# Kernel tuning notes

Hardware: AMD Instinct MI355X
Metric: run time of the kernel (lower is better)

The kernel has to match this reference:

```python
import jax, jax.numpy as jnp
import numpy as np

NUM_USERS = 100000
NUM_ITEMS = 50000
EMBED = 64
S_NNZ = NUM_USERS * 32   # avg social degree 32
R_NNZ = NUM_USERS * 50   # avg 50 rated items per user
BATCH = 8192


def setup_inputs() -> dict:
    key = jax.random.key(0)
    ks = jax.random.split(key, 12)
    d = EMBED
    # Embedding tables (xavier-uniform style scale)
    U = jax.random.uniform(ks[0], (NUM_USERS, d), jnp.float32, -1.0, 1.0) * np.sqrt(6.0 / (NUM_USERS + d))
    V = jax.random.uniform(ks[1], (NUM_ITEMS, d), jnp.float32, -1.0, 1.0) * np.sqrt(6.0 / (NUM_ITEMS + d))
    # Diffusion layer weights: Linear(2d -> d). Stored as [2d, d] (x @ W + b).
    lim = np.sqrt(6.0 / (3 * d))
    W0 = jax.random.uniform(ks[2], (2 * d, d), jnp.float32, -lim, lim)
    b0 = jnp.zeros((d,), jnp.float32)
    W1 = jax.random.uniform(ks[3], (2 * d, d), jnp.float32, -lim, lim)
    b1 = jnp.zeros((d,), jnp.float32)
    # Sparse social matrix S [NUM_USERS, NUM_USERS], COO edge lists, row-normalized values.
    S_row = jax.random.randint(ks[4], (S_NNZ,), 0, NUM_USERS, jnp.int32)
    S_col = jax.random.randint(ks[5], (S_NNZ,), 0, NUM_USERS, jnp.int32)
    S_val = jnp.full((S_NNZ,), 1.0 / 32.0, jnp.float32)
    # Sparse rating matrix R [NUM_USERS, NUM_ITEMS]
    R_row = jax.random.randint(ks[6], (R_NNZ,), 0, NUM_USERS, jnp.int32)
    R_col = jax.random.randint(ks[7], (R_NNZ,), 0, NUM_ITEMS, jnp.int32)
    R_val = jnp.full((R_NNZ,), 1.0 / 50.0, jnp.float32)
    batch_user = jax.random.randint(ks[8], (BATCH,), 0, NUM_USERS, jnp.int64 if jax.config.jax_enable_x64 else jnp.int32)
    batch_pos_item = jax.random.randint(ks[9], (BATCH,), 0, NUM_ITEMS, jnp.int32)
    batch_neg_item = jax.random.randint(ks[10], (BATCH,), 0, NUM_ITEMS, jnp.int32)
    return dict(batch_user=batch_user, batch_pos_item=batch_pos_item, batch_neg_item=batch_neg_item,
                U=U, V=V, W0=W0, b0=b0, W1=W1, b1=b1,
                S_row=S_row, S_col=S_col, S_val=S_val,
                R_row=R_row, R_col=R_col, R_val=R_val)


def _spmm(row, col, val, X, n_rows):
    # (sparse [n_rows, n] COO) @ X : gather + scale + segment-sum
    return jax.ops.segment_sum(val[:, None] * X[col], row, num_segments=n_rows)


def reference(batch_user, batch_pos_item, batch_neg_item, U, V, W0, b0, W1, b1,
              S_row, S_col, S_val, R_row, R_col, R_val):
    # Diffusion layers: U <- relu(concat([S @ U, U]) @ W + b)
    for W, b in ((W0, b0), (W1, b1)):
        agg = _spmm(S_row, S_col, S_val, U, NUM_USERS)          # [num_users, d]
        U = jax.nn.relu(jnp.concatenate([agg, U], axis=1) @ W + b)
    user_g = U + _spmm(R_row, R_col, R_val, V, NUM_USERS)        # [num_users, d]
    bu = user_g[batch_user]          # [B, d]
    bp = V[batch_pos_item]           # [B, d]
    bn = V[batch_neg_item]           # [B, d]
    return (bu, bp, bn)
```

## Files before the change

### kernel.cpp

```cpp
#include <hip/hip_runtime.h>
#include <hip/hip_bf16.h>

#define NUM_USERS 100000
#define NUM_ITEMS 50000
#define EMBED     64
#define S_NNZ     (NUM_USERS * 32)
#define R_NNZ     (NUM_USERS * 50)
#define BATCH     8192

#define NB    256
#define NCH   256
#define CHUNK (S_NNZ / NCH)
#define BROWS 391

#define SEGCAP 160


__global__ __launch_bounds__(256) void k_p1hist(const int* __restrict__ rows, int* __restrict__ cnt_t,
                                                int* __restrict__ head, unsigned* __restrict__ bitmap,
                                                int* __restrict__ cntR) {
    __shared__ int h[NB];
    int t = threadIdx.x, b = blockIdx.x;
    int gid = b * 256 + t;
    for (int i = gid; i < NUM_USERS; i += NB * 256) head[i] = -1;
    for (int i = gid; i < (NUM_USERS + 31) / 32; i += NB * 256) bitmap[i] = 0;
    for (int i = gid; i < BATCH; i += NB * 256) cntR[i] = 0;
    h[t] = 0;
    __syncthreads();
    int base = b * CHUNK;
    for (int i = t; i < CHUNK; i += 256) atomicAdd(&h[rows[base + i] / BROWS], 1);
    __syncthreads();
    cnt_t[t * NCH + b] = h[t];
}

__global__ __launch_bounds__(1024) void k_scan1(const int* __restrict__ cnt, int* __restrict__ excl,
                                                int* __restrict__ bsums, int n) {
    __shared__ int buf[1024];
    int t = threadIdx.x;
    int i = blockIdx.x * 1024 + t;
    int x = (i < n) ? cnt[i] : 0;
    buf[t] = x;
    __syncthreads();
    for (int off = 1; off < 1024; off <<= 1) {
        int y = (t >= off) ? buf[t - off] : 0;
        __syncthreads();
        buf[t] += y;
        __syncthreads();
    }
    if (i < n) excl[i] = buf[t] - x;
    if (t == 1023) bsums[blockIdx.x] = buf[1023];
}

__global__ __launch_bounds__(1024) void k_scan2(int* __restrict__ bsums, int nb, int* __restrict__ total_slot) {
    __shared__ int buf[1024];
    int t = threadIdx.x;
    int x = (t < nb) ? bsums[t] : 0;
    buf[t] = x;
    __syncthreads();
    for (int off = 1; off < 1024; off <<= 1) {
        int y = (t >= off) ? buf[t - off] : 0;
        __syncthreads();
        buf[t] += y;
        __syncthreads();
    }
    if (t < nb) bsums[t] = buf[t] - x;
    if (t == 1023) total_slot[0] = buf[1023];
}

__global__ void k_scan3b(int* __restrict__ a, const int* __restrict__ bsums, int n) {
    int i = blockIdx.x * blockDim.x + threadIdx.x;
    if (i < n) a[i] += bsums[i >> 10];
}

__global__ __launch_bounds__(256) void k_p1scatter(const int* __restrict__ rows, const int* __restrict__ cols,
                                                   const float* __restrict__ vals, const int* __restrict__ cnt_t,
                                                   int2* __restrict__ tmpE) {
    __shared__ int cur[NB];
    int t = threadIdx.x, b = blockIdx.x;
    cur[t] = cnt_t[t * NCH + b];
    __syncthreads();
    int base = b * CHUNK;
    for (int i = t; i < CHUNK; i += 256) {
        int e  = base + i;
        int r  = rows[e];
        int bk = r / BROWS;
        int pos = atomicAdd(&cur[bk], 1);
        tmpE[pos] = make_int2(((r - bk * BROWS) << 17) | cols[e], __float_as_int(vals[e]));
    }
}

__global__ __launch_bounds__(512) void k_p2(const int2* __restrict__ tmpE, const int* __restrict__ cnt_t,
                                            int* __restrict__ rowptr, int2* __restrict__ colval) {
    __shared__ int h[512];
    __shared__ int s[512];
    __shared__ int cur[512];
    int t = threadIdx.x, k = blockIdx.x;
    int beg = cnt_t[k * NCH];
    int end = (k < NB - 1) ? cnt_t[(k + 1) * NCH] : S_NNZ;
    h[t] = 0;
    __syncthreads();
    for (int j = beg + t; j < end; j += 512) atomicAdd(&h[((unsigned)tmpE[j].x) >> 17], 1);
    __syncthreads();
    s[t] = h[t];
    __syncthreads();
    for (int off = 1; off < 512; off <<= 1) {
        int y = (t >= off) ? s[t - off] : 0;
        __syncthreads();
        s[t] += y;
        __syncthreads();
    }
    int excl = s[t] - h[t];
    int gr   = k * BROWS + t;
    if (t <= BROWS && gr <= NUM_USERS) rowptr[gr] = beg + excl;
    cur[t] = beg + excl;
    __syncthreads();
    for (int j = beg + t; j < end; j += 512) {
        int2 e  = tmpE[j];
        int pos = atomicAdd(&cur[((unsigned)e.x) >> 17], 1);
        colval[pos] = make_int2(e.x & 0x1FFFF, e.y);
    }
}

__global__ void k_cvt(const float* __restrict__ src, __hip_bfloat16* __restrict__ dst, int n) {
    int i = blockIdx.x * blockDim.x + threadIdx.x;
    if (i < n) dst[i] = __float2bfloat16(src[i]);
}

__global__ __launch_bounds__(256) void k_spmm16(const int* __restrict__ rowptr,
                                                const int2* __restrict__ colval,
                                                const __hip_bfloat16* __restrict__ X,
                                                float* __restrict__ Y, int n_rows) {
    int w    = blockIdx.x * (blockDim.x >> 6) + (threadIdx.x >> 6);
    int lane = threadIdx.x & 63;
    if (w >= n_rows) return;
    int beg = rowptr[w], end = rowptr[w + 1];
    float acc = 0.0f;
    int j    = beg;
    int jend = beg + ((end - beg) & ~7);
    for (; j < jend; j += 8) {
        int2 cv[8];
#pragma unroll
        for (int u = 0; u < 8; ++u) cv[u] = colval[j + u];
        float x[8];
#pragma unroll
        for (int u = 0; u < 8; ++u) x[u] = __bfloat162float(X[(size_t)cv[u].x * EMBED + lane]);
#pragma unroll
        for (int u = 0; u < 8; ++u) acc = fmaf(__int_as_float(cv[u].y), x[u], acc);
    }
    for (; j < end; ++j)
        acc = fmaf(__int_as_float(colval[j].y), __bfloat162float(X[(size_t)colval[j].x * EMBED + lane]), acc);
    Y[(size_t)w * EMBED + lane] = acc;
}

__global__ __launch_bounds__(256) void k_spmm_batch16(const int* __restrict__ rowptr,
                                                      const int2* __restrict__ colval,
                                                      const __hip_bfloat16* __restrict__ X,
                                                      const int* __restrict__ bu,
                                                      float* __restrict__ Agg2, int n) {
    int w    = blockIdx.x * (blockDim.x >> 6) + (threadIdx.x >> 6);
    int lane = threadIdx.x & 63;
    if (w >= n) return;
    int r   = bu[w];
    int beg = rowptr[r], end = rowptr[r + 1];
    float acc = 0.0f;
    int j    = beg;
    int jend = beg + ((end - beg) & ~7);
    for (; j < jend; j += 8) {
        int2 cv[8];
#pragma unroll
        for (int u = 0; u < 8; ++u) cv[u] = colval[j + u];
        float x[8];
#pragma unroll
        for (int u = 0; u < 8; ++u) x[u] = __bfloat162float(X[(size_t)cv[u].x * EMBED + lane]);
#pragma unroll
        for (int u = 0; u < 8; ++u) acc = fmaf(__int_as_float(cv[u].y), x[u], acc);
    }
    for (; j < end; ++j)
        acc = fmaf(__int_as_float(colval[j].y), __bfloat162float(X[(size_t)colval[j].x * EMBED + lane]), acc);
    Agg2[(size_t)w * EMBED + lane] = acc;
}


__global__ __launch_bounds__(256) void k_layer(const float* __restrict__ Agg,
                                               const float* __restrict__ Uin,
                                               float* __restrict__ Uout,
                                               __hip_bfloat16* __restrict__ Uout16,
                                               const float* __restrict__ W,
                                               const float* __restrict__ b) {
    __shared__ __align__(16) float Wt[64 * 128];
    int t = threadIdx.x;
    for (int i = t; i < 128 * 64; i += 256) {
        int k = i >> 6, c = i & 63;
        Wt[c * 128 + ((((k >> 2) ^ (c & 7)) << 2) | (k & 3))] = W[i];
    }
    int rl = __builtin_amdgcn_readfirstlane(t >> 6);
    int c  = t & 63;
    int rbase = blockIdx.x * 16 + rl * 4;
    __syncthreads();
    const float4* Wt4 = (const float4*)Wt;
    int  csw   = c & 7;
    int  cbase = c * 32;
    const float4* a0 = (const float4*)(Agg + (size_t)(rbase + 0) * EMBED);
    const float4* a1 = (const float4*)(Agg + (size_t)(rbase + 1) * EMBED);
    const float4* a2 = (const float4*)(Agg + (size_t)(rbase + 2) * EMBED);
    const float4* a3 = (const float4*)(Agg + (size_t)(rbase + 3) * EMBED);
    const float4* u0 = (const float4*)(Uin + (size_t)(rbase + 0) * EMBED);
    const float4* u1 = (const float4*)(Uin + (size_t)(rbase + 1) * EMBED);
    const float4* u2 = (const float4*)(Uin + (size_t)(rbase + 2) * EMBED);
    const float4* u3 = (const float4*)(Uin + (size_t)(rbase + 3) * EMBED);
    float bias = b[c];
    float acc0 = bias, acc1 = bias, acc2 = bias, acc3 = bias;
#pragma unroll 4
    for (int k4 = 0; k4 < 16; ++k4) {
        float4 w4 = Wt4[cbase + (k4 ^ csw)];
        float4 x0 = a0[k4], x1 = a1[k4], x2 = a2[k4], x3 = a3[k4];
        acc0 = fmaf(x0.x, w4.x, acc0); acc0 = fmaf(x0.y, w4.y, acc0); acc0 = fmaf(x0.z, w4.z, acc0); acc0 = fmaf(x0.w, w4.w, acc0);
        acc1 = fmaf(x1.x, w4.x, acc1); acc1 = fmaf(x1.y, w4.y, acc1); acc1 = fmaf(x1.z, w4.z, acc1); acc1 = fmaf(x1.w, w4.w, acc1);
        acc2 = fmaf(x2.x, w4.x, acc2); acc2 = fmaf(x2.y, w4.y, acc2); acc2 = fmaf(x2.z, w4.z, acc2); acc2 = fmaf(x2.w, w4.w, acc2);
        acc3 = fmaf(x3.x, w4.x, acc3); acc3 = fmaf(x3.y, w4.y, acc3); acc3 = fmaf(x3.z, w4.z, acc3); acc3 = fmaf(x3.w, w4.w, acc3);
    }
#pragma unroll 4
    for (int k4 = 16; k4 < 32; ++k4) {
        float4 w4 = Wt4[cbase + (k4 ^ csw)];
        float4 x0 = u0[k4 - 16], x1 = u1[k4 - 16], x2 = u2[k4 - 16], x3 = u3[k4 - 16];
        acc0 = fmaf(x0.x, w4.x, acc0); acc0 = fmaf(x0.y, w4.y, acc0); acc0 = fmaf(x0.z, w4.z, acc0); acc0 = fmaf(x0.w, w4.w, acc0);
        acc1 = fmaf(x1.x, w4.x, acc1); acc1 = fmaf(x1.y, w4.y, acc1); acc1 = fmaf(x1.z, w4.z, acc1); acc1 = fmaf(x1.w, w4.w, acc1);
        acc2 = fmaf(x2.x, w4.x, acc2); acc2 = fmaf(x2.y, w4.y, acc2); acc2 = fmaf(x2.z, w4.z, acc2); acc2 = fmaf(x2.w, w4.w, acc2);
        acc3 = fmaf(x3.x, w4.x, acc3); acc3 = fmaf(x3.y, w4.y, acc3); acc3 = fmaf(x3.z, w4.z, acc3); acc3 = fmaf(x3.w, w4.w, acc3);
    }
    float v0 = fmaxf(acc0, 0.0f), v1 = fmaxf(acc1, 0.0f), v2 = fmaxf(acc2, 0.0f), v3 = fmaxf(acc3, 0.0f);
    Uout[(size_t)(rbase + 0) * EMBED + c] = v0;
    Uout[(size_t)(rbase + 1) * EMBED + c] = v1;
    Uout[(size_t)(rbase + 2) * EMBED + c] = v2;
    Uout[(size_t)(rbase + 3) * EMBED + c] = v3;
    Uout16[(size_t)(rbase + 0) * EMBED + c] = __float2bfloat16(v0);
    Uout16[(size_t)(rbase + 1) * EMBED + c] = __float2bfloat16(v1);
    Uout16[(size_t)(rbase + 2) * EMBED + c] = __float2bfloat16(v2);
    Uout16[(size_t)(rbase + 3) * EMBED + c] = __float2bfloat16(v3);
}

__global__ __launch_bounds__(256) void k_layer_batch(const float* __restrict__ Agg2,
                                                     const float* __restrict__ Uin,
                                                     const int* __restrict__ bu,
                                                     float* __restrict__ out0,
                                                     const float* __restrict__ W,
                                                     const float* __restrict__ b,
                                                     const float* __restrict__ V,
                                                     const int* __restrict__ bp,
                                                     const int* __restrict__ bn) {
    __shared__ __align__(16) float Wt[64 * 128];
    int t = threadIdx.x;
    for (int i = t; i < 128 * 64; i += 256) {
        int k = i >> 6, c = i & 63;
        Wt[c * 128 + ((((k >> 2) ^ (c & 7)) << 2) | (k & 3))] = W[i];
    }
    int rl = __builtin_amdgcn_readfirstlane(t >> 6);
    int c  = t & 63;
    int sbase = blockIdx.x * 16 + rl * 4;
    int r0 = bu[sbase + 0], r1 = bu[sbase + 1], r2 = bu[sbase + 2], r3 = bu[sbase + 3];
    __syncthreads();
    const float4* Wt4 = (const float4*)Wt;
    int  csw   = c & 7;
    int  cbase = c * 32;
    const float4* a0 = (const float4*)(Agg2 + (size_t)(sbase + 0) * EMBED);
    const float4* a1 = (const float4*)(Agg2 + (size_t)(sbase + 1) * EMBED);
    const float4* a2 = (const float4*)(Agg2 + (size_t)(sbase + 2) * EMBED);
    const float4* a3 = (const float4*)(Agg2 + (size_t)(sbase + 3) * EMBED);
    const float4* u0 = (const float4*)(Uin + (size_t)r0 * EMBED);
    const float4* u1 = (const float4*)(Uin + (size_t)r1 * EMBED);
    const float4* u2 = (const float4*)(Uin + (size_t)r2 * EMBED);
    const float4* u3 = (const float4*)(Uin + (size_t)r3 * EMBED);
    float bias = b[c];
    float acc0 = bias, acc1 = bias, acc2 = bias, acc3 = bias;
#pragma unroll 4
    for (int k4 = 0; k4 < 16; ++k4) {
        float4 w4 = Wt4[cbase + (k4 ^ csw)];
        float4 x0 = a0[k4], x1 = a1[k4], x2 = a2[k4], x3 = a3[k4];
        acc0 = fmaf(x0.x, w4.x, acc0); acc0 = fmaf(x0.y, w4.y, acc0); acc0 = fmaf(x0.z, w4.z, acc0); acc0 = fmaf(x0.w, w4.w, acc0);
        acc1 = fmaf(x1.x, w4.x, acc1); acc1 = fmaf(x1.y, w4.y, acc1); acc1 = fmaf(x1.z, w4.z, acc1); acc1 = fmaf(x1.w, w4.w, acc1);
        acc2 = fmaf(x2.x, w4.x, acc2); acc2 = fmaf(x2.y, w4.y, acc2); acc2 = fmaf(x2.z, w4.z, acc2); acc2 = fmaf(x2.w, w4.w, acc2);
        acc3 = fmaf(x3.x, w4.x, acc3); acc3 = fmaf(x3.y, w4.y, acc3); acc3 = fmaf(x3.z, w4.z, acc3); acc3 = fmaf(x3.w, w4.w, acc3);
    }
#pragma unroll 4
    for (int k4 = 16; k4 < 32; ++k4) {
        float4 w4 = Wt4[cbase + (k4 ^ csw)];
        float4 x0 = u0[k4 - 16], x1 = u1[k4 - 16], x2 = u2[k4 - 16], x3 = u3[k4 - 16];
        acc0 = fmaf(x0.x, w4.x, acc0); acc0 = fmaf(x0.y, w4.y, acc0); acc0 = fmaf(x0.z, w4.z, acc0); acc0 = fmaf(x0.w, w4.w, acc0);
        acc1 = fmaf(x1.x, w4.x, acc1); acc1 = fmaf(x1.y, w4.y, acc1); acc1 = fmaf(x1.z, w4.z, acc1); acc1 = fmaf(x1.w, w4.w, acc1);
        acc2 = fmaf(x2.x, w4.x, acc2); acc2 = fmaf(x2.y, w4.y, acc2); acc2 = fmaf(x2.z, w4.z, acc2); acc2 = fmaf(x2.w, w4.w, acc2);
        acc3 = fmaf(x3.x, w4.x, acc3); acc3 = fmaf(x3.y, w4.y, acc3); acc3 = fmaf(x3.z, w4.z, acc3); acc3 = fmaf(x3.w, w4.w, acc3);
    }
    out0[(size_t)(sbase + 0) * EMBED + c] = fmaxf(acc0, 0.0f);
    out0[(size_t)(sbase + 1) * EMBED + c] = fmaxf(acc1, 0.0f);
    out0[(size_t)(sbase + 2) * EMBED + c] = fmaxf(acc2, 0.0f);
    out0[(size_t)(sbase + 3) * EMBED + c] = fmaxf(acc3, 0.0f);
#pragma unroll
    for (int q = 0; q < 4; ++q) {
        int s = sbase + q;
        out0[(size_t)(BATCH + s) * EMBED + c]     = V[(size_t)bp[s] * EMBED + c];
        out0[(size_t)(2 * BATCH + s) * EMBED + c] = V[(size_t)bn[s] * EMBED + c];
    }
}


__global__ void k_chain(const int* __restrict__ bu, int* __restrict__ head,
                        int* __restrict__ nxt, unsigned* __restrict__ bitmap, int n) {
    int i = blockIdx.x * blockDim.x + threadIdx.x;
    if (i < n) {
        int u = bu[i];
        nxt[i] = atomicExch(&head[u], i);
        atomicOr(&bitmap[u >> 5], 1u << (u & 31));
    }
}

__global__ __launch_bounds__(256) void k_rseg(const int* __restrict__ rows,
                                              const int* __restrict__ cols,
                                              const float* __restrict__ vals,
                                              const unsigned* __restrict__ bitmap,
                                              const int* __restrict__ head,
                                              int* __restrict__ cntR,
                                              int2* __restrict__ seg, int nnz,
                                              const float* __restrict__ V,
                                              __hip_bfloat16* __restrict__ V16) {
    int e = blockIdx.x * blockDim.x + threadIdx.x;
    if (e < NUM_ITEMS * EMBED) V16[e] = __float2bfloat16(V[e]);
    if (e >= nnz) return;
    int r = rows[e];
    if (!((bitmap[(unsigned)r >> 5] >> (r & 31)) & 1u)) return;
    int s   = head[r];
    int pos = atomicAdd(&cntR[s], 1);
    if (pos < SEGCAP) seg[s * SEGCAP + pos] = make_int2(cols[e], __float_as_int(vals[e]));
}

__global__ __launch_bounds__(256) void k_rspmm(const int* __restrict__ cntR,
                                               const int2* __restrict__ seg,
                                               const __hip_bfloat16* __restrict__ V16,
                                               const int* __restrict__ bu,
                                               const int* __restrict__ head,
                                               const int* __restrict__ nxt,
                                               float* __restrict__ out0) {
    int s    = blockIdx.x * (blockDim.x >> 6) + (threadIdx.x >> 6);
    int lane = threadIdx.x & 63;
    if (s >= BATCH) return;
    if (head[bu[s]] != s) return;
    int n = cntR[s];
    if (n > SEGCAP) n = SEGCAP;
    const int2* cv2 = seg + (size_t)s * SEGCAP;
    float acc = 0.0f;
    int j    = 0;
    int jend = n & ~7;
    for (; j < jend; j += 8) {
        int2 cv[8];
#pragma unroll
        for (int u = 0; u < 8; ++u) cv[u] = cv2[j + u];
        float x[8];
#pragma unroll
        for (int u = 0; u < 8; ++u) x[u] = __bfloat162float(V16[(size_t)cv[u].x * EMBED + lane]);
#pragma unroll
        for (int u = 0; u < 8; ++u) acc = fmaf(__int_as_float(cv[u].y), x[u], acc);
    }
    for (; j < n; ++j)
        acc = fmaf(__int_as_float(cv2[j].y), __bfloat162float(V16[(size_t)cv2[j].x * EMBED + lane]), acc);
    int slot = s;
    while (slot >= 0) {
        out0[(size_t)slot * EMBED + lane] += acc;
        slot = nxt[slot];
    }
}


extern "C" void kernel_launch(void* const* d_in, const int* in_sizes, int n_in,
                              void* d_out, int out_size, void* d_ws, size_t ws_size,
                              hipStream_t stream) {
    const int*   batch_user = (const int*)d_in[0];
    const int*   batch_pos  = (const int*)d_in[1];
    const int*   batch_neg  = (const int*)d_in[2];
    const float* U     = (const float*)d_in[3];
    const float* V     = (const float*)d_in[4];
    const float* W0    = (const float*)d_in[5];
    const float* b0    = (const float*)d_in[6];
    const float* W1    = (const float*)d_in[7];
    const float* b1    = (const float*)d_in[8];
    const int*   S_row = (const int*)d_in[9];
    const int*   S_col = (const int*)d_in[10];
    const float* S_val = (const float*)d_in[11];
    const int*   R_row = (const int*)d_in[12];
    const int*   R_col = (const int*)d_in[13];
    const float* R_val = (const float*)d_in[14];
    float* out = (float*)d_out;

    const size_t tabElems = (size_t)NUM_USERS * EMBED;

    char* wsb = (char*)d_ws;
    size_t o = 0;
    float* A       = (float*)(wsb + o); o += tabElems * 4;
    float* B       = (float*)(wsb + o); o += tabElems * 4;
    float* Agg2    = (float*)(wsb + o); o += (size_t)BATCH * EMBED * 4;
    int*   rowptrS = (int*)(wsb + o);   o += (NUM_USERS + 1) * 4;
    int*   cnt_t   = (int*)(wsb + o);   o += (size_t)NB * NCH * 4;
    int*   bsums   = (int*)(wsb + o);   o += 1024 * 4;
    int*   head    = (int*)(wsb + o);   o += NUM_USERS * 4;
    int*   nxt     = (int*)(wsb + o);   o += BATCH * 4;
    int*   cntR    = (int*)(wsb + o);   o += BATCH * 4;
    unsigned* bitmap = (unsigned*)(wsb + o); o += ((NUM_USERS + 31) / 32) * 4;
    o = (o + 7) & ~(size_t)7;
    int2*  colvalS = (int2*)(wsb + o);  o += (size_t)S_NNZ * 8;
    __hip_bfloat16* X16 = (__hip_bfloat16*)(wsb + o); o += tabElems * 2;

    int2* tmpE = (int2*)A;
    int2* seg  = (int2*)B;

    const int spmm_blocks  = (NUM_USERS * 64 + 255) / 256;
    const int layer_blocks = (NUM_USERS + 15) / 16;

    k_p1hist<<<NCH, 256, 0, stream>>>(S_row, cnt_t, head, bitmap, cntR);
    k_scan1<<<(NB * NCH) / 1024, 1024, 0, stream>>>(cnt_t, cnt_t, bsums, NB * NCH);
    k_scan2<<<1, 1024, 0, stream>>>(bsums, (NB * NCH) / 1024, &bsums[512]);
    k_scan3b<<<(NB * NCH) / 256, 256, 0, stream>>>(cnt_t, bsums, NB * NCH);
    k_p1scatter<<<NCH, 256, 0, stream>>>(S_row, S_col, S_val, cnt_t, tmpE);
    k_p2<<<NB, 512, 0, stream>>>(tmpE, cnt_t, rowptrS, colvalS);

    k_cvt<<<(int)((tabElems + 255) / 256), 256, 0, stream>>>(U, X16, (int)tabElems);
    k_spmm16<<<spmm_blocks, 256, 0, stream>>>(rowptrS, colvalS, X16, B, NUM_USERS);
    k_layer<<<layer_blocks, 256, 0, stream>>>(B, U, A, X16, W0, b0);

    k_chain<<<(BATCH + 255) / 256, 256, 0, stream>>>(batch_user, head, nxt, bitmap, BATCH);

    k_spmm_batch16<<<(BATCH * 64 + 255) / 256, 256, 0, stream>>>(rowptrS, colvalS, X16, batch_user, Agg2, BATCH);
    k_layer_batch<<<(BATCH + 15) / 16, 256, 0, stream>>>(Agg2, A, batch_user, out, W1, b1,
                                                         V, batch_pos, batch_neg);

    k_rseg<<<(R_NNZ + 255) / 256, 256, 0, stream>>>(R_row, R_col, R_val, bitmap, head, cntR, seg, R_NNZ,
                                                    V, X16);
    k_rspmm<<<(BATCH * 64 + 255) / 256, 256, 0, stream>>>(cntR, seg, X16, batch_user, head, nxt, out);
}
```

Baseline: 511.6 us.

## Fuse SpMM with dense layer and fold small kernels into preprocessing

Merges the social SpMM and the Linear+ReLU layer into one kernel, for both the full-table layer and the batch-only second layer. Each wave computes the aggregated row, stages it with the input row in LDS, and multiplies by the LDS-resident weight matrix. This removes the fp32 Agg round trip through global memory and several launches. The batch chain-building work is folded into k_scan1 and the fp32-to-bf16 conversion of U into k_p1scatter. The cost is more LDS per block, lower occupancy with 512-thread blocks, and per-row serialization of the gather and the matmul within a wave.

```diff
diff --git a/kernel.cpp b/kernel.cpp
--- a/kernel.cpp
+++ b/kernel.cpp
@@ -34,10 +34,17 @@
 }
 
 __global__ __launch_bounds__(1024) void k_scan1(const int* __restrict__ cnt, int* __restrict__ excl,
-                                                int* __restrict__ bsums, int n) {
-    __shared__ int buf[1024];
+                                                int* __restrict__ bsums, int n,
+                                                const int* __restrict__ bu, int* __restrict__ head,
+                                                int* __restrict__ nxt, unsigned* __restrict__ bitmap) {
     int t = threadIdx.x;
     int i = blockIdx.x * 1024 + t;
+    if (i < BATCH) {
+        int u = bu[i];
+        nxt[i] = atomicExch(&head[u], i);
+        atomicOr(&bitmap[u >> 5], 1u << (u & 31));
+    }
+    __shared__ int buf[1024];
     int x = (i < n) ? cnt[i] : 0;
     buf[t] = x;
     __syncthreads();
@@ -74,7 +81,8 @@
 
 __global__ __launch_bounds__(256) void k_p1scatter(const int* __restrict__ rows, const int* __restrict__ cols,
                                                    const float* __restrict__ vals, const int* __restrict__ cnt_t,
-                                                   int2* __restrict__ tmpE) {
+                                                   int2* __restrict__ tmpE,
+                                                   const float* __restrict__ U, __hip_bfloat16* __restrict__ U16) {
     __shared__ int cur[NB];
     int t = threadIdx.x, b = blockIdx.x;
     cur[t] = cnt_t[t * NCH + b];
@@ -87,6 +95,8 @@
         int pos = atomicAdd(&cur[bk], 1);
         tmpE[pos] = make_int2(((r - bk * BROWS) << 17) | cols[e], __float_as_int(vals[e]));
     }
+    const int total = NUM_USERS * EMBED;
+    for (int i = b * 256 + t; i < total; i += NB * 256) U16[i] = __float2bfloat16(U[i]);
 }
 
 __global__ __launch_bounds__(512) void k_p2(const int2* __restrict__ tmpE, const int* __restrict__ cnt_t,
@@ -121,197 +131,129 @@
     }
 }
 
-__global__ void k_cvt(const float* __restrict__ src, __hip_bfloat16* __restrict__ dst, int n) {
-    int i = blockIdx.x * blockDim.x + threadIdx.x;
-    if (i < n) dst[i] = __float2bfloat16(src[i]);
-}
-
-__global__ __launch_bounds__(256) void k_spmm16(const int* __restrict__ rowptr,
-                                                const int2* __restrict__ colval,
-                                                const __hip_bfloat16* __restrict__ X,
-                                                float* __restrict__ Y, int n_rows) {
-    int w    = blockIdx.x * (blockDim.x >> 6) + (threadIdx.x >> 6);
-    int lane = threadIdx.x & 63;
-    if (w >= n_rows) return;
-    int beg = rowptr[w], end = rowptr[w + 1];
-    float acc = 0.0f;
-    int j    = beg;
-    int jend = beg + ((end - beg) & ~7);
-    for (; j < jend; j += 8) {
-        int2 cv[8];
-#pragma unroll
-        for (int u = 0; u < 8; ++u) cv[u] = colval[j + u];
-        float x[8];
-#pragma unroll
-        for (int u = 0; u < 8; ++u) x[u] = __bfloat162float(X[(size_t)cv[u].x * EMBED + lane]);
-#pragma unroll
-        for (int u = 0; u < 8; ++u) acc = fmaf(__int_as_float(cv[u].y), x[u], acc);
-    }
-    for (; j < end; ++j)
-        acc = fmaf(__int_as_float(colval[j].y), __bfloat162float(X[(size_t)colval[j].x * EMBED + lane]), acc);
-    Y[(size_t)w * EMBED + lane] = acc;
-}
-
-__global__ __launch_bounds__(256) void k_spmm_batch16(const int* __restrict__ rowptr,
-                                                      const int2* __restrict__ colval,
-                                                      const __hip_bfloat16* __restrict__ X,
-                                                      const int* __restrict__ bu,
-                                                      float* __restrict__ Agg2, int n) {
-    int w    = blockIdx.x * (blockDim.x >> 6) + (threadIdx.x >> 6);
-    int lane = threadIdx.x & 63;
-    if (w >= n) return;
-    int r   = bu[w];
-    int beg = rowptr[r], end = rowptr[r + 1];
-    float acc = 0.0f;
-    int j    = beg;
-    int jend = beg + ((end - beg) & ~7);
-    for (; j < jend; j += 8) {
-        int2 cv[8];
-#pragma unroll
-        for (int u = 0; u < 8; ++u) cv[u] = colval[j + u];
-        float x[8];
-#pragma unroll
-        for (int u = 0; u < 8; ++u) x[u] = __bfloat162float(X[(size_t)cv[u].x * EMBED + lane]);
-#pragma unroll
-        for (int u = 0; u < 8; ++u) acc = fmaf(__int_as_float(cv[u].y), x[u], acc);
-    }
-    for (; j < end; ++j)
-        acc = fmaf(__int_as_float(colval[j].y), __bfloat162float(X[(size_t)colval[j].x * EMBED + lane]), acc);
-    Agg2[(size_t)w * EMBED + lane] = acc;
-}
-
-
-__global__ __launch_bounds__(256) void k_layer(const float* __restrict__ Agg,
-                                               const float* __restrict__ Uin,
-                                               float* __restrict__ Uout,
-                                               __hip_bfloat16* __restrict__ Uout16,
-                                               const float* __restrict__ W,
-                                               const float* __restrict__ b) {
-    __shared__ __align__(16) float Wt[64 * 128];
+
+__global__ __launch_bounds__(512) void k_spmm_layer(const int* __restrict__ rowptr,
+                                                    const int2* __restrict__ colval,
+                                                    const __hip_bfloat16* __restrict__ X,
+                                                    const float* __restrict__ Uin,
+                                                    float* __restrict__ Uout,
+                                                    __hip_bfloat16* __restrict__ Uout16,
+                                                    const float* __restrict__ W,
+                                                    const float* __restrict__ b) {
+    __shared__ __align__(16) float Wl[128 * 64];
+    __shared__ __align__(16) float xs[8][128];
     int t = threadIdx.x;
-    for (int i = t; i < 128 * 64; i += 256) {
+    for (int i = t; i < 128 * 64; i += 512) {
         int k = i >> 6, c = i & 63;
-        Wt[c * 128 + ((((k >> 2) ^ (c & 7)) << 2) | (k & 3))] = W[i];
-    }
-    int rl = __builtin_amdgcn_readfirstlane(t >> 6);
-    int c  = t & 63;
-    int rbase = blockIdx.x * 16 + rl * 4;
-    __syncthreads();
-    const float4* Wt4 = (const float4*)Wt;
-    int  csw   = c & 7;
-    int  cbase = c * 32;
-    const float4* a0 = (const float4*)(Agg + (size_t)(rbase + 0) * EMBED);
-    const float4* a1 = (const float4*)(Agg + (size_t)(rbase + 1) * EMBED);
-    const float4* a2 = (const float4*)(Agg + (size_t)(rbase + 2) * EMBED);
-    const float4* a3 = (const float4*)(Agg + (size_t)(rbase + 3) * EMBED);
-    const float4* u0 = (const float4*)(Uin + (size_t)(rbase + 0) * EMBED);
-    const float4* u1 = (const float4*)(Uin + (size_t)(rbase + 1) * EMBED);
-    const float4* u2 = (const float4*)(Uin + (size_t)(rbase + 2) * EMBED);
-    const float4* u3 = (const float4*)(Uin + (size_t)(rbase + 3) * EMBED);
-    float bias = b[c];
-    float acc0 = bias, acc1 = bias, acc2 = bias, acc3 = bias;
-#pragma unroll 4
-    for (int k4 = 0; k4 < 16; ++k4) {
-        float4 w4 = Wt4[cbase + (k4 ^ csw)];
-        float4 x0 = a0[k4], x1 = a1[k4], x2 = a2[k4], x3 = a3[k4];
-        acc0 = fmaf(x0.x, w4.x, acc0); acc0 = fmaf(x0.y, w4.y, acc0); acc0 = fmaf(x0.z, w4.z, acc0); acc0 = fmaf(x0.w, w4.w, acc0);
-        acc1 = fmaf(x1.x, w4.x, acc1); acc1 = fmaf(x1.y, w4.y, acc1); acc1 = fmaf(x1.z, w4.z, acc1); acc1 = fmaf(x1.w, w4.w, acc1);
-        acc2 = fmaf(x2.x, w4.x, acc2); acc2 = fmaf(x2.y, w4.y, acc2); acc2 = fmaf(x2.z, w4.z, acc2); acc2 = fmaf(x2.w, w4.w, acc2);
-        acc3 = fmaf(x3.x, w4.x, acc3); acc3 = fmaf(x3.y, w4.y, acc3); acc3 = fmaf(x3.z, w4.z, acc3); acc3 = fmaf(x3.w, w4.w, acc3);
-    }
-#pragma unroll 4
-    for (int k4 = 16; k4 < 32; ++k4) {
-        float4 w4 = Wt4[cbase + (k4 ^ csw)];
-        float4 x0 = u0[k4 - 16], x1 = u1[k4 - 16], x2 = u2[k4 - 16], x3 = u3[k4 - 16];
-        acc0 = fmaf(x0.x, w4.x, acc0); acc0 = fmaf(x0.y, w4.y, acc0); acc0 = fmaf(x0.z, w4.z, acc0); acc0 = fmaf(x0.w, w4.w, acc0);
-        acc1 = fmaf(x1.x, w4.x, acc1); acc1 = fmaf(x1.y, w4.y, acc1); acc1 = fmaf(x1.z, w4.z, acc1); acc1 = fmaf(x1.w, w4.w, acc1);
-        acc2 = fmaf(x2.x, w4.x, acc2); acc2 = fmaf(x2.y, w4.y, acc2); acc2 = fmaf(x2.z, w4.z, acc2); acc2 = fmaf(x2.w, w4.w, acc2);
-        acc3 = fmaf(x3.x, w4.x, acc3); acc3 = fmaf(x3.y, w4.y, acc3); acc3 = fmaf(x3.z, w4.z, acc3); acc3 = fmaf(x3.w, w4.w, acc3);
-    }
-    float v0 = fmaxf(acc0, 0.0f), v1 = fmaxf(acc1, 0.0f), v2 = fmaxf(acc2, 0.0f), v3 = fmaxf(acc3, 0.0f);
-    Uout[(size_t)(rbase + 0) * EMBED + c] = v0;
-    Uout[(size_t)(rbase + 1) * EMBED + c] = v1;
-    Uout[(size_t)(rbase + 2) * EMBED + c] = v2;
-    Uout[(size_t)(rbase + 3) * EMBED + c] = v3;
-    Uout16[(size_t)(rbase + 0) * EMBED + c] = __float2bfloat16(v0);
-    Uout16[(size_t)(rbase + 1) * EMBED + c] = __float2bfloat16(v1);
-    Uout16[(size_t)(rbase + 2) * EMBED + c] = __float2bfloat16(v2);
-    Uout16[(size_t)(rbase + 3) * EMBED + c] = __float2bfloat16(v3);
-}
-
-__global__ __launch_bounds__(256) void k_layer_batch(const float* __restrict__ Agg2,
-                                                     const float* __restrict__ Uin,
-                                                     const int* __restrict__ bu,
-                                                     float* __restrict__ out0,
-                                                     const float* __restrict__ W,
-                                                     const float* __restrict__ b,
-                                                     const float* __restrict__ V,
-                                                     const int* __restrict__ bp,
-                                                     const int* __restrict__ bn) {
-    __shared__ __align__(16) float Wt[64 * 128];
+        Wl[c * 128 + ((((k >> 2) ^ (c & 7)) << 2) | (k & 3))] = W[i];
+    }
+    __syncthreads();
+    int wv   = t >> 6;
+    int lane = t & 63;
+    int csw  = lane & 7;
+    int cbase = lane * 32;
+    const float4* Wt4 = (const float4*)Wl;
+    float bias = b[lane];
+    int rbase = blockIdx.x * 32 + wv * 4;
+#pragma unroll
+    for (int q = 0; q < 4; ++q) {
+        int row = rbase + q;
+        int beg = rowptr[row], end = rowptr[row + 1];
+        float acc = 0.0f;
+        int j    = beg;
+        int jend = beg + ((end - beg) & ~7);
+        for (; j < jend; j += 8) {
+            int2 cv[8];
+#pragma unroll
+            for (int u = 0; u < 8; ++u) cv[u] = colval[j + u];
+            float x[8];
+#pragma unroll
+            for (int u = 0; u < 8; ++u) x[u] = __bfloat162float(X[(size_t)cv[u].x * EMBED + lane]);
+#pragma unroll
+            for (int u = 0; u < 8; ++u) acc = fmaf(__int_as_float(cv[u].y), x[u], acc);
+        }
+        for (; j < end; ++j)
+            acc = fmaf(__int_as_float(colval[j].y), __bfloat162float(X[(size_t)colval[j].x * EMBED + lane]), acc);
+        xs[wv][lane]      = acc;
+        xs[wv][64 + lane] = Uin[(size_t)row * EMBED + lane];
+        const float4* xv = (const float4*)xs[wv];
+        float accL = bias;
+#pragma unroll 8
+        for (int k4 = 0; k4 < 32; ++k4) {
+            float4 w4 = Wt4[cbase + (k4 ^ csw)];
+            float4 x4 = xv[k4];
+            accL = fmaf(x4.x, w4.x, accL); accL = fmaf(x4.y, w4.y, accL);
+            accL = fmaf(x4.z, w4.z, accL); accL = fmaf(x4.w, w4.w, accL);
+        }
+        float v = fmaxf(accL, 0.0f);
+        Uout[(size_t)row * EMBED + lane]   = v;
+        Uout16[(size_t)row * EMBED + lane] = __float2bfloat16(v);
+    }
+}
+
+__global__ __launch_bounds__(512) void k_spmm_layer_batch(const int* __restrict__ rowptr,
+                                                          const int2* __restrict__ colval,
+                                                          const __hip_bfloat16* __restrict__ X,
+                                                          const float* __restrict__ Uin,
+                                                          const int* __restrict__ bu,
+                                                          float* __restrict__ out0,
+                                                          const float* __restrict__ W,
+                                                          const float* __restrict__ b,
+                                                          const float* __restrict__ V,
+                                                          const int* __restrict__ bp,
+                                                          const int* __restrict__ bn) {
+    __shared__ __align__(16) float Wl[128 * 64];
+    __shared__ __align__(16) float xs[8][128];
     int t = threadIdx.x;
-    for (int i = t; i < 128 * 64; i += 256) {
+    for (int i = t; i < 128 * 64; i += 512) {
         int k = i >> 6, c = i & 63;
-        Wt[c * 128 + ((((k >> 2) ^ (c & 7)) << 2) | (k & 3))] = W[i];
-    }
-    int rl = __builtin_amdgcn_readfirstlane(t >> 6);
-    int c  = t & 63;
-    int sbase = blockIdx.x * 16 + rl * 4;
-    int r0 = bu[sbase + 0], r1 = bu[sbase + 1], r2 = bu[sbase + 2], r3 = bu[sbase + 3];
-    __syncthreads();
-    const float4* Wt4 = (const float4*)Wt;
-    int  csw   = c & 7;
-    int  cbase = c * 32;
-    const float4* a0 = (const float4*)(Agg2 + (size_t)(sbase + 0) * EMBED);
-    const float4* a1 = (const float4*)(Agg2 + (size_t)(sbase + 1) * EMBED);
-    const float4* a2 = (const float4*)(Agg2 + (size_t)(sbase + 2) * EMBED);
-    const float4* a3 = (const float4*)(Agg2 + (size_t)(sbase + 3) * EMBED);
-    const float4* u0 = (const float4*)(Uin + (size_t)r0 * EMBED);
-    const float4* u1 = (const float4*)(Uin + (size_t)r1 * EMBED);
-    const float4* u2 = (const float4*)(Uin + (size_t)r2 * EMBED);
-    const float4* u3 = (const float4*)(Uin + (size_t)r3 * EMBED);
-    float bias = b[c];
-    float acc0 = bias, acc1 = bias, acc2 = bias, acc3 = bias;
-#pragma unroll 4
-    for (int k4 = 0; k4 < 16; ++k4) {
-        float4 w4 = Wt4[cbase + (k4 ^ csw)];
-        float4 x0 = a0[k4], x1 = a1[k4], x2 = a2[k4], x3 = a3[k4];
-        acc0 = fmaf(x0.x, w4.x, acc0); acc0 = fmaf(x0.y, w4.y, acc0); acc0 = fmaf(x0.z, w4.z, acc0); acc0 = fmaf(x0.w, w4.w, acc0);
-        acc1 = fmaf(x1.x, w4.x, acc1); acc1 = fmaf(x1.y, w4.y, acc1); acc1 = fmaf(x1.z, w4.z, acc1); acc1 = fmaf(x1.w, w4.w, acc1);
-        acc2 = fmaf(x2.x, w4.x, acc2); acc2 = fmaf(x2.y, w4.y, acc2); acc2 = fmaf(x2.z, w4.z, acc2); acc2 = fmaf(x2.w, w4.w, acc2);
-        acc3 = fmaf(x3.x, w4.x, acc3); acc3 = fmaf(x3.y, w4.y, acc3); acc3 = fmaf(x3.z, w4.z, acc3); acc3 = fmaf(x3.w, w4.w, acc3);
-    }
-#pragma unroll 4
-    for (int k4 = 16; k4 < 32; ++k4) {
-        float4 w4 = Wt4[cbase + (k4 ^ csw)];
-        float4 x0 = u0[k4 - 16], x1 = u1[k4 - 16], x2 = u2[k4 - 16], x3 = u3[k4 - 16];
-        acc0 = fmaf(x0.x, w4.x, acc0); acc0 = fmaf(x0.y, w4.y, acc0); acc0 = fmaf(x0.z, w4.z, acc0); acc0 = fmaf(x0.w, w4.w, acc0);
-        acc1 = fmaf(x1.x, w4.x, acc1); acc1 = fmaf(x1.y, w4.y, acc1); acc1 = fmaf(x1.z, w4.z, acc1); acc1 = fmaf(x1.w, w4.w, acc1);
-        acc2 = fmaf(x2.x, w4.x, acc2); acc2 = fmaf(x2.y, w4.y, acc2); acc2 = fmaf(x2.z, w4.z, acc2); acc2 = fmaf(x2.w, w4.w, acc2);
-        acc3 = fmaf(x3.x, w4.x, acc3); acc3 = fmaf(x3.y, w4.y, acc3); acc3 = fmaf(x3.z, w4.z, acc3); acc3 = fmaf(x3.w, w4.w, acc3);
-    }
-    out0[(size_t)(sbase + 0) * EMBED + c] = fmaxf(acc0, 0.0f);
-    out0[(size_t)(sbase + 1) * EMBED + c] = fmaxf(acc1, 0.0f);
-    out0[(size_t)(sbase + 2) * EMBED + c] = fmaxf(acc2, 0.0f);
-    out0[(size_t)(sbase + 3) * EMBED + c] = fmaxf(acc3, 0.0f);
+        Wl[c * 128 + ((((k >> 2) ^ (c & 7)) << 2) | (k & 3))] = W[i];
+    }
+    __syncthreads();
+    int wv   = t >> 6;
+    int lane = t & 63;
+    int csw  = lane & 7;
+    int cbase = lane * 32;
+    const float4* Wt4 = (const float4*)Wl;
+    float bias = b[lane];
+    int sbase = blockIdx.x * 32 + wv * 4;
 #pragma unroll
     for (int q = 0; q < 4; ++q) {
         int s = sbase + q;
-        out0[(size_t)(BATCH + s) * EMBED + c]     = V[(size_t)bp[s] * EMBED + c];
-        out0[(size_t)(2 * BATCH + s) * EMBED + c] = V[(size_t)bn[s] * EMBED + c];
-    }
-}
-
-
-__global__ void k_chain(const int* __restrict__ bu, int* __restrict__ head,
-                        int* __restrict__ nxt, unsigned* __restrict__ bitmap, int n) {
-    int i = blockIdx.x * blockDim.x + threadIdx.x;
-    if (i < n) {
-        int u = bu[i];
-        nxt[i] = atomicExch(&head[u], i);
-        atomicOr(&bitmap[u >> 5], 1u << (u & 31));
-    }
-}
+        int r = bu[s];
+        int beg = rowptr[r], end = rowptr[r + 1];
+        float acc = 0.0f;
+        int j    = beg;
+        int jend = beg + ((end - beg) & ~7);
+        for (; j < jend; j += 8) {
+            int2 cv[8];
+#pragma unroll
+            for (int u = 0; u < 8; ++u) cv[u] = colval[j + u];
+            float x[8];
+#pragma unroll
+            for (int u = 0; u < 8; ++u) x[u] = __bfloat162float(X[(size_t)cv[u].x * EMBED + lane]);
+#pragma unroll
+            for (int u = 0; u < 8; ++u) acc = fmaf(__int_as_float(cv[u].y), x[u], acc);
+        }
+        for (; j < end; ++j)
+            acc = fmaf(__int_as_float(colval[j].y), __bfloat162float(X[(size_t)colval[j].x * EMBED + lane]), acc);
+        xs[wv][lane]      = acc;
+        xs[wv][64 + lane] = Uin[(size_t)r * EMBED + lane];
+        const float4* xv = (const float4*)xs[wv];
+        float accL = bias;
+#pragma unroll 8
+        for (int k4 = 0; k4 < 32; ++k4) {
+            float4 w4 = Wt4[cbase + (k4 ^ csw)];
+            float4 x4 = xv[k4];
+            accL = fmaf(x4.x, w4.x, accL); accL = fmaf(x4.y, w4.y, accL);
+            accL = fmaf(x4.z, w4.z, accL); accL = fmaf(x4.w, w4.w, accL);
+        }
+        out0[(size_t)s * EMBED + lane] = fmaxf(accL, 0.0f);
+        out0[(size_t)(BATCH + s) * EMBED + lane]     = V[(size_t)bp[s] * EMBED + lane];
+        out0[(size_t)(2 * BATCH + s) * EMBED + lane] = V[(size_t)bn[s] * EMBED + lane];
+    }
+}
+
 
 __global__ __launch_bounds__(256) void k_rseg(const int* __restrict__ rows,
                                               const int* __restrict__ cols,
@@ -395,7 +337,6 @@
     size_t o = 0;
     float* A       = (float*)(wsb + o); o += tabElems * 4;
     float* B       = (float*)(wsb + o); o += tabElems * 4;
-    float* Agg2    = (float*)(wsb + o); o += (size_t)BATCH * EMBED * 4;
     int*   rowptrS = (int*)(wsb + o);   o += (NUM_USERS + 1) * 4;
     int*   cnt_t   = (int*)(wsb + o);   o += (size_t)NB * NCH * 4;
     int*   bsums   = (int*)(wsb + o);   o += 1024 * 4;
@@ -409,26 +350,20 @@
 
     int2* tmpE = (int2*)A;
     int2* seg  = (int2*)B;
-
-    const int spmm_blocks  = (NUM_USERS * 64 + 255) / 256;
-    const int layer_blocks = (NUM_USERS + 15) / 16;
+    __hip_bfloat16* A16 = (__hip_bfloat16*)((char*)B + tabElems * 2);
 
     k_p1hist<<<NCH, 256, 0, stream>>>(S_row, cnt_t, head, bitmap, cntR);
-    k_scan1<<<(NB * NCH) / 1024, 1024, 0, stream>>>(cnt_t, cnt_t, bsums, NB * NCH);
+    k_scan1<<<(NB * NCH) / 1024, 1024, 0, stream>>>(cnt_t, cnt_t, bsums, NB * NCH,
+                                                    batch_user, head, nxt, bitmap);
     k_scan2<<<1, 1024, 0, stream>>>(bsums, (NB * NCH) / 1024, &bsums[512]);
     k_scan3b<<<(NB * NCH) / 256, 256, 0, stream>>>(cnt_t, bsums, NB * NCH);
-    k_p1scatter<<<NCH, 256, 0, stream>>>(S_row, S_col, S_val, cnt_t, tmpE);
+    k_p1scatter<<<NCH, 256, 0, stream>>>(S_row, S_col, S_val, cnt_t, tmpE, U, X16);
     k_p2<<<NB, 512, 0, stream>>>(tmpE, cnt_t, rowptrS, colvalS);
 
-    k_cvt<<<(int)((tabElems + 255) / 256), 256, 0, stream>>>(U, X16, (int)tabElems);
-    k_spmm16<<<spmm_blocks, 256, 0, stream>>>(rowptrS, colvalS, X16, B, NUM_USERS);
-    k_layer<<<layer_blocks, 256, 0, stream>>>(B, U, A, X16, W0, b0);
-
-    k_chain<<<(BATCH + 255) / 256, 256, 0, stream>>>(batch_user, head, nxt, bitmap, BATCH);
-
-    k_spmm_batch16<<<(BATCH * 64 + 255) / 256, 256, 0, stream>>>(rowptrS, colvalS, X16, batch_user, Agg2, BATCH);
-    k_layer_batch<<<(BATCH + 15) / 16, 256, 0, stream>>>(Agg2, A, batch_user, out, W1, b1,
-                                                         V, batch_pos, batch_neg);
+    k_spmm_layer<<<NUM_USERS / 32, 512, 0, stream>>>(rowptrS, colvalS, X16, U, A, A16, W0, b0);
+
+    k_spmm_layer_batch<<<BATCH / 32, 512, 0, stream>>>(rowptrS, colvalS, A16, A, batch_user,
+                                                       out, W1, b1, V, batch_pos, batch_neg);
 
     k_rseg<<<(R_NNZ + 255) / 256, 256, 0, stream>>>(R_row, R_col, R_val, bitmap, head, cntR, seg, R_NNZ,
                                                     V, X16);
```

Measured after the change: 578.2 us. +13.0%, slower.
